# Kernel tuning notes

Measured on AMD Instinct MI355X. Metric: run time of the kernel, lower is better.

The kernel has to match this reference:

```python
import jax, jax.numpy as jnp
import numpy as np

MARGIN = 0.3
BIG = 10000.0  # sentinel used by the original when a gt/lt negative set is empty


def setup_inputs() -> dict:
    key = jax.random.key(0)
    k1, k2 = jax.random.split(key)
    inputs = jax.random.normal(k1, (4096, 256), dtype=jnp.float32)
    targets = jax.random.randint(k2, (4096,), 0, 4, dtype=jnp.int32)
    return {"inputs": inputs, "targets": targets}


def reference(inputs, targets):
    # Pairwise Euclidean distance matrix (n, n).
    sq = jnp.sum(inputs * inputs, axis=1)
    d2 = sq[:, None] + sq[None, :] - 2.0 * (inputs @ inputs.T)
    dist = jnp.sqrt(jnp.maximum(d2, 0.0))

    # mask[i, j] semantics from the torch code (rows of expand are `targets`):
    #   eq: targets[j] == targets[i]; gt: targets[j] > targets[i]; lt: targets[j] < targets[i]
    eq = targets[None, :] == targets[:, None]
    gt = targets[None, :] > targets[:, None]
    lt = targets[None, :] < targets[:, None]

    # Hardest positive: max distance over same-label columns (diag always eq -> non-empty).
    hard_ap = jnp.max(jnp.where(eq, dist, -jnp.inf), axis=1)
    # Hardest greater / less negatives: min distance, sentinel BIG when set empty.
    an_g = jnp.min(jnp.where(gt, dist, jnp.inf), axis=1)
    an_g = jnp.where(jnp.isinf(an_g), BIG, an_g)
    an_l = jnp.min(jnp.where(lt, dist, jnp.inf), axis=1)
    an_l = jnp.where(jnp.isinf(an_l), BIG, an_l)

    loss = jnp.mean(jax.nn.relu(hard_ap - jnp.abs(an_g - an_l) + MARGIN))
    # cnt: rows whose positive set is just the anchor itself
    cnt = jnp.sum(jnp.sum(eq, axis=1) == 1)
    return loss, dist, cnt
```

## Files before the change

kernel.cpp:

```cpp
#include <hip/hip_runtime.h>

#define N 4096
#define D 256
#define MARGIN 0.3f
#define BIG 10000.0f

typedef _Float16 f16x8 __attribute__((ext_vector_type(8)));
typedef _Float16 f16x4 __attribute__((ext_vector_type(4)));
typedef float floatx16 __attribute__((ext_vector_type(16)));

__device__ inline void atomicMaxFloatPos(float* a, float v) {
    atomicMax((int*)a, __float_as_int(v));
}
__device__ inline void atomicMinFloatPos(float* a, float v) {
    atomicMin((int*)a, __float_as_int(v));
}

__device__ inline void gl_lds16(const void* g, void* l) {
    __builtin_amdgcn_global_load_lds(
        (const __attribute__((address_space(1))) unsigned int*)g,
        (__attribute__((address_space(3))) unsigned int*)l, 16, 0, 0);
}

__global__ __launch_bounds__(256) void prep_kernel(const float* __restrict__ x,
                                                   float* __restrict__ sq,
                                                   _Float16* __restrict__ Xf,
                                                   float* ap, float* ang, float* anl) {
    const int wave = threadIdx.x >> 6, lane = threadIdx.x & 63;
    const int row = blockIdx.x * 4 + wave;
    const float4 v = *(const float4*)(x + (size_t)row * D + lane * 4);
    f16x4 h;
    h[0] = (_Float16)v.x; h[1] = (_Float16)v.y;
    h[2] = (_Float16)v.z; h[3] = (_Float16)v.w;
    *(f16x4*)(Xf + (size_t)row * D + lane * 4) = h;
    const float c0 = (float)h[0], c1 = (float)h[1], c2 = (float)h[2], c3 = (float)h[3];
    float s = c0 * c0 + c1 * c1 + c2 * c2 + c3 * c3;
    #pragma unroll
    for (int off = 32; off; off >>= 1) s += __shfl_down(s, off);
    if (lane == 0) sq[row] = s;
    if (threadIdx.x < 4) {
        const int i = blockIdx.x * 4 + threadIdx.x;
        ap[i] = 0.0f; ang[i] = BIG; anl[i] = BIG;
    }
}

__global__ __launch_bounds__(64) void dist_kernel(const _Float16* __restrict__ Xf,
                                                  const int* __restrict__ tgt,
                                                  const float* __restrict__ sq,
                                                  float* __restrict__ dist,
                                                  float* ap, float* ang, float* anl) {
    __shared__ _Float16 lds[4096];

    const int lane = threadIdx.x;
    const int row0 = blockIdx.y * 64;
    const int col0 = blockIdx.x * 64;

    const int g  = lane >> 3;
    const int p  = lane & 7;
    const int lq = p ^ g;
    const _Float16* src0 = Xf + (size_t)((lq < 4 ? row0 : col0) + g) * D + (lq & 3) * 8;

    floatx16 acc[2][2];
    #pragma unroll
    for (int mt = 0; mt < 2; ++mt)
        #pragma unroll
        for (int nt = 0; nt < 2; ++nt)
            #pragma unroll
            for (int r = 0; r < 16; ++r) acc[mt][nt][r] = 0.0f;

    const int m0 = lane & 31;
    const int hi = lane >> 5;
    const int sw = m0 & 7;

    #pragma unroll
    for (int s = 0; s < 8; ++s) {
        const int k0 = s * 32;
        __asm__ volatile("s_waitcnt lgkmcnt(0)" ::: "memory");
        #pragma unroll
        for (int d = 0; d < 8; ++d)
            gl_lds16(src0 + (size_t)d * 8 * D + k0, lds + d * 512);
        __asm__ volatile("s_waitcnt vmcnt(0)" ::: "memory");

        __builtin_amdgcn_s_setprio(1);
        #pragma unroll
        for (int ks = 0; ks < 2; ++ks) {
            const int la = ks * 2 + hi;
            f16x8 a0 = *(const f16x8*)(lds + m0 * 64        + ((la ^ sw) << 3));
            f16x8 a1 = *(const f16x8*)(lds + (32 + m0) * 64 + ((la ^ sw) << 3));
            f16x8 b0 = *(const f16x8*)(lds + m0 * 64        + (((4 + la) ^ sw) << 3));
            f16x8 b1 = *(const f16x8*)(lds + (32 + m0) * 64 + (((4 + la) ^ sw) << 3));
            acc[0][0] = __builtin_amdgcn_mfma_f32_32x32x16_f16(a0, b0, acc[0][0], 0, 0, 0);
            acc[0][1] = __builtin_amdgcn_mfma_f32_32x32x16_f16(a0, b1, acc[0][1], 0, 0, 0);
            acc[1][0] = __builtin_amdgcn_mfma_f32_32x32x16_f16(a1, b0, acc[1][0], 0, 0, 0);
            acc[1][1] = __builtin_amdgcn_mfma_f32_32x32x16_f16(a1, b1, acc[1][1], 0, 0, 0);
        }
        __builtin_amdgcn_s_setprio(0);
        __asm__ volatile("" ::: "memory");
    }

    const int tl = tgt[row0 + lane];
    const unsigned long long pb0 = __ballot(tl & 1);
    const unsigned long long pb1 = __ballot(tl & 2);
    const int tc0 = tgt[col0 + m0], tc1 = tgt[col0 + 32 + m0];
    const int gc0 = col0 + m0,      gc1 = col0 + 32 + m0;
    const float sqc0 = sq[gc0], sqc1 = sq[gc1];
    const int rl_base = 4 * hi;

    float mx0 = 0.0f, mg0 = BIG, ml0 = BIG;
    float mx1 = 0.0f, mg1 = BIG, ml1 = BIG;

    #pragma unroll
    for (int mt = 0; mt < 2; ++mt) {
        #pragma unroll
        for (int r = 0; r < 16; ++r) {
            const int row_l = mt * 32 + (r & 3) + 8 * (r >> 2) + rl_base;
            const int grow  = row0 + row_l;
            const float sqi = sq[grow];
            const float d0 = sqrtf(fmaxf(sqi + sqc0 - 2.0f * acc[mt][0][r], 0.0f));
            const float d1 = sqrtf(fmaxf(sqi + sqc1 - 2.0f * acc[mt][1][r], 0.0f));
            __builtin_nontemporal_store(d0, dist + (size_t)grow * N + gc0);
            __builtin_nontemporal_store(d1, dist + (size_t)grow * N + gc1);
            const int tr = (int)((pb0 >> row_l) & 1) | ((int)((pb1 >> row_l) & 1) << 1);
            mx0 = fmaxf(mx0, (tr == tc0) ? d0 : 0.0f);
            mg0 = fminf(mg0, (tr >  tc0) ? d0 : BIG);
            ml0 = fminf(ml0, (tr <  tc0) ? d0 : BIG);
            mx1 = fmaxf(mx1, (tr == tc1) ? d1 : 0.0f);
            mg1 = fminf(mg1, (tr >  tc1) ? d1 : BIG);
            ml1 = fminf(ml1, (tr <  tc1) ? d1 : BIG);
        }
    }
    mx0 = fmaxf(mx0, __shfl_xor(mx0, 32));
    mg0 = fminf(mg0, __shfl_xor(mg0, 32));
    ml0 = fminf(ml0, __shfl_xor(ml0, 32));
    mx1 = fmaxf(mx1, __shfl_xor(mx1, 32));
    mg1 = fminf(mg1, __shfl_xor(mg1, 32));
    ml1 = fminf(ml1, __shfl_xor(ml1, 32));

    if (hi == 0) {
        atomicMaxFloatPos(&ap[gc0],  mx0);
        atomicMinFloatPos(&ang[gc0], mg0);
        atomicMinFloatPos(&anl[gc0], ml0);
        atomicMaxFloatPos(&ap[gc1],  mx1);
        atomicMinFloatPos(&ang[gc1], mg1);
        atomicMinFloatPos(&anl[gc1], ml1);
    }
}

__global__ __launch_bounds__(1024) void finish_kernel(const float* __restrict__ ap,
                                                      const float* __restrict__ ang,
                                                      const float* __restrict__ anl,
                                                      const int* __restrict__ tgt,
                                                      float* __restrict__ out) {
    __shared__ int hist[4];
    __shared__ unsigned hsum[2][16];
    __shared__ float wsum[16];
    __shared__ int wcnt[16];
    const int tid = threadIdx.x, lane = tid & 63, wv = tid >> 6;

    const int4 t4 = *(const int4*)&tgt[tid * 4];
    int c[4] = {0, 0, 0, 0};
    c[t4.x & 3]++; c[t4.y & 3]++; c[t4.z & 3]++; c[t4.w & 3]++;
    unsigned p01 = (unsigned)c[0] | ((unsigned)c[1] << 16);
    unsigned p23 = (unsigned)c[2] | ((unsigned)c[3] << 16);
    #pragma unroll
    for (int off = 32; off; off >>= 1) {
        p01 += __shfl_down(p01, off);
        p23 += __shfl_down(p23, off);
    }
    if (lane == 0) { hsum[0][wv] = p01; hsum[1][wv] = p23; }
    __syncthreads();
    if (tid == 0) {
        unsigned a = 0, b = 0;
        for (int i = 0; i < 16; ++i) { a += hsum[0][i]; b += hsum[1][i]; }
        hist[0] = a & 0xFFFF; hist[1] = a >> 16;
        hist[2] = b & 0xFFFF; hist[3] = b >> 16;
    }
    __syncthreads();

    float term = 0.0f; int cc = 0;
    const int lab[4] = {t4.x & 3, t4.y & 3, t4.z & 3, t4.w & 3};
    #pragma unroll
    for (int j = 0; j < 4; ++j) {
        const int i = tid * 4 + j;
        term += fmaxf(ap[i] - fabsf(ang[i] - anl[i]) + MARGIN, 0.0f);
        cc += (hist[lab[j]] == 1) ? 1 : 0;
    }
    #pragma unroll
    for (int off = 32; off; off >>= 1) {
        term += __shfl_down(term, off);
        cc   += __shfl_down(cc, off);
    }
    if (lane == 0) { wsum[wv] = term; wcnt[wv] = cc; }
    __syncthreads();
    if (tid == 0) {
        float ls = 0.0f; int cs = 0;
        for (int i = 0; i < 16; ++i) { ls += wsum[i]; cs += wcnt[i]; }
        out[0] = ls * (1.0f / N);
        out[1 + (size_t)N * N] = (float)cs;
    }
}

extern "C" void kernel_launch(void* const* d_in, const int* in_sizes, int n_in,
                              void* d_out, int out_size, void* d_ws, size_t ws_size,
                              hipStream_t stream) {
    const float* x   = (const float*)d_in[0];
    const int*   tgt = (const int*)d_in[1];
    float* out = (float*)d_out;
    char*  ws  = (char*)d_ws;

    _Float16* Xf  = (_Float16*)ws;
    float*    sq  = (float*)(ws + 2097152);
    float*    ap  = sq + 4096;
    float*    ang = sq + 8192;
    float*    anl = sq + 12288;

    prep_kernel<<<N / 4, 256, 0, stream>>>(x, sq, Xf, ap, ang, anl);
    dim3 grid(N / 64, N / 64);
    dist_kernel<<<grid, 64, 0, stream>>>(Xf, tgt, sq, out + 1, ap, ang, anl);
    finish_kernel<<<1, 1024, 0, stream>>>(ap, ang, anl, tgt, out);
}
```

Baseline: 120.2 us.

## Use 128x128 block tiles with four waves sharing LDS operand tiles

The distance kernel moves from one 64-wave block per 64x64 tile to 256-thread blocks covering 128x128 tiles. Each wave loads a quarter of the A/B panels into shared LDS with a K-step of 64, and barriers coordinate the waves. This halves the global reads of X per output element and takes the per-row sq loads out of the epilogue by shuffling them from a register. The cost is barrier synchronization and larger LDS use, which can limit occupancy. The kernel is likely bound by writing the 64MB distance matrix anyway.

New measurement: 113.2 us. 1.06x faster.

```diff
diff --git a/kernel.cpp b/kernel.cpp
--- a/kernel.cpp
+++ b/kernel.cpp
@@ -44,21 +44,37 @@
     }
 }
 
-__global__ __launch_bounds__(64) void dist_kernel(const _Float16* __restrict__ Xf,
-                                                  const int* __restrict__ tgt,
-                                                  const float* __restrict__ sq,
-                                                  float* __restrict__ dist,
-                                                  float* ap, float* ang, float* anl) {
-    __shared__ _Float16 lds[4096];
-
-    const int lane = threadIdx.x;
-    const int row0 = blockIdx.y * 64;
-    const int col0 = blockIdx.x * 64;
-
-    const int g  = lane >> 3;
-    const int p  = lane & 7;
-    const int lq = p ^ g;
-    const _Float16* src0 = Xf + (size_t)((lq < 4 ? row0 : col0) + g) * D + (lq & 3) * 8;
+__global__ __launch_bounds__(256, 4) void dist_kernel(const _Float16* __restrict__ Xf,
+                                                      const int* __restrict__ tgt,
+                                                      const float* __restrict__ sq,
+                                                      float* __restrict__ dist,
+                                                      float* ap, float* ang, float* anl) {
+    __shared__ _Float16 lds[16384];
+
+    const int tid  = threadIdx.x;
+    const int wv   = tid >> 6;
+    const int lane = tid & 63;
+    const int row0 = blockIdx.y * 128;
+    const int col0 = blockIdx.x * 128;
+    const int wr = wv >> 1, wc = wv & 1;
+
+    const int g = lane >> 3, p = lane & 7, lq = p ^ g;
+    const int selrow = (wv < 2 ? row0 : col0) + (wv & 1) * 64 + g;
+    const _Float16* src0 = Xf + (size_t)selrow * D + lq * 8;
+    _Float16* dst0 = lds + wv * 8 * 512;
+
+    const int m0 = lane & 31;
+    const int hi = lane >> 5;
+    const int sw = m0 & 7;
+    const int rowbase = row0 + wr * 64;
+    const int colbase = col0 + wc * 64;
+    const int tl = tgt[rowbase + lane];
+    const float sq_r = sq[rowbase + lane];
+    const unsigned long long pb0 = __ballot(tl & 1);
+    const unsigned long long pb1 = __ballot(tl & 2);
+    const int gc0 = colbase + m0, gc1 = colbase + 32 + m0;
+    const int tc0 = tgt[gc0], tc1 = tgt[gc1];
+    const float sqc0 = sq[gc0], sqc1 = sq[gc1];
 
     floatx16 acc[2][2];
     #pragma unroll
@@ -68,27 +84,33 @@
             #pragma unroll
             for (int r = 0; r < 16; ++r) acc[mt][nt][r] = 0.0f;
 
-    const int m0 = lane & 31;
-    const int hi = lane >> 5;
-    const int sw = m0 & 7;
-
-    #pragma unroll
-    for (int s = 0; s < 8; ++s) {
-        const int k0 = s * 32;
-        __asm__ volatile("s_waitcnt lgkmcnt(0)" ::: "memory");
+    const _Float16* ldsA0 = lds + (wr * 64 + m0) * 64;
+    const _Float16* ldsA1 = lds + (wr * 64 + 32 + m0) * 64;
+    const _Float16* ldsB0 = lds + 8192 + (wc * 64 + m0) * 64;
+    const _Float16* ldsB1 = lds + 8192 + (wc * 64 + 32 + m0) * 64;
+
+    #pragma unroll
+    for (int s = 0; s < 4; ++s) {
+        if (s) {
+            __asm__ volatile("s_waitcnt lgkmcnt(0)" ::: "memory");
+            __builtin_amdgcn_s_barrier();
+        }
+        const int k0 = s * 64;
         #pragma unroll
         for (int d = 0; d < 8; ++d)
-            gl_lds16(src0 + (size_t)d * 8 * D + k0, lds + d * 512);
+            gl_lds16(src0 + (size_t)d * 8 * D + k0, dst0 + d * 512);
         __asm__ volatile("s_waitcnt vmcnt(0)" ::: "memory");
+        __builtin_amdgcn_s_barrier();
 
         __builtin_amdgcn_s_setprio(1);
         #pragma unroll
-        for (int ks = 0; ks < 2; ++ks) {
+        for (int ks = 0; ks < 4; ++ks) {
             const int la = ks * 2 + hi;
-            f16x8 a0 = *(const f16x8*)(lds + m0 * 64        + ((la ^ sw) << 3));
-            f16x8 a1 = *(const f16x8*)(lds + (32 + m0) * 64 + ((la ^ sw) << 3));
-            f16x8 b0 = *(const f16x8*)(lds + m0 * 64        + (((4 + la) ^ sw) << 3));
-            f16x8 b1 = *(const f16x8*)(lds + (32 + m0) * 64 + (((4 + la) ^ sw) << 3));
+            const int po = (la ^ sw) << 3;
+            f16x8 a0 = *(const f16x8*)(ldsA0 + po);
+            f16x8 a1 = *(const f16x8*)(ldsA1 + po);
+            f16x8 b0 = *(const f16x8*)(ldsB0 + po);
+            f16x8 b1 = *(const f16x8*)(ldsB1 + po);
             acc[0][0] = __builtin_amdgcn_mfma_f32_32x32x16_f16(a0, b0, acc[0][0], 0, 0, 0);
             acc[0][1] = __builtin_amdgcn_mfma_f32_32x32x16_f16(a0, b1, acc[0][1], 0, 0, 0);
             acc[1][0] = __builtin_amdgcn_mfma_f32_32x32x16_f16(a1, b0, acc[1][0], 0, 0, 0);
@@ -98,12 +120,6 @@
         __asm__ volatile("" ::: "memory");
     }
 
-    const int tl = tgt[row0 + lane];
-    const unsigned long long pb0 = __ballot(tl & 1);
-    const unsigned long long pb1 = __ballot(tl & 2);
-    const int tc0 = tgt[col0 + m0], tc1 = tgt[col0 + 32 + m0];
-    const int gc0 = col0 + m0,      gc1 = col0 + 32 + m0;
-    const float sqc0 = sq[gc0], sqc1 = sq[gc1];
     const int rl_base = 4 * hi;
 
     float mx0 = 0.0f, mg0 = BIG, ml0 = BIG;
@@ -114,8 +130,8 @@
         #pragma unroll
         for (int r = 0; r < 16; ++r) {
             const int row_l = mt * 32 + (r & 3) + 8 * (r >> 2) + rl_base;
-            const int grow  = row0 + row_l;
-            const float sqi = sq[grow];
+            const int grow  = rowbase + row_l;
+            const float sqi = __shfl(sq_r, row_l);
             const float d0 = sqrtf(fmaxf(sqi + sqc0 - 2.0f * acc[mt][0][r], 0.0f));
             const float d1 = sqrtf(fmaxf(sqi + sqc1 - 2.0f * acc[mt][1][r], 0.0f));
             __builtin_nontemporal_store(d0, dist + (size_t)grow * N + gc0);
@@ -215,7 +231,7 @@
     float*    anl = sq + 12288;
 
     prep_kernel<<<N / 4, 256, 0, stream>>>(x, sq, Xf, ap, ang, anl);
-    dim3 grid(N / 64, N / 64);
-    dist_kernel<<<grid, 64, 0, stream>>>(Xf, tgt, sq, out + 1, ap, ang, anl);
+    dim3 grid(N / 128, N / 128);
+    dist_kernel<<<grid, 256, 0, stream>>>(Xf, tgt, sq, out + 1, ap, ang, anl);
     finish_kernel<<<1, 1024, 0, stream>>>(ap, ang, anl, tgt, out);
 }
```
